# Optimization experiments

Hardware: AMD Instinct MI355X
Metric: run time of the kernel (lower is better)

## Reference

```python
import jax, jax.numpy as jnp
import numpy as np

E = 1024   # embedding_dim
H = 16     # heads
W = 1024   # lag / seq length
B = 4      # batch
D = E // H # head dim


def setup_inputs() -> dict:
    key = jax.random.key(0)
    ks = jax.random.split(key, 5)
    scale = E ** -0.5
    return {
        "x":   jax.random.normal(ks[0], (3, B, E, W), dtype=jnp.float32),
        "L_Q": jax.random.normal(ks[1], (E, E), dtype=jnp.float32) * scale,
        "L_K": jax.random.normal(ks[2], (E, E), dtype=jnp.float32) * scale,
        "L_V": jax.random.normal(ks[3], (E, E), dtype=jnp.float32) * scale,
        "M":   jax.random.normal(ks[4], (E, E), dtype=jnp.float32) * (1.0 / (2 * E)) ** 0.5,
        "b":   jnp.zeros((E, 1), dtype=jnp.float32),
    }


def reference(x, L_Q, L_K, L_V, M, b):
    # x: [3, B, E, W] channels-first; x[0]=K input, x[1]=Q input, x[2]=V input
    K = jnp.einsum('ef,bfw->bew', L_K, x[0])
    Q = jnp.einsum('ef,bfw->bew', L_Q, x[1])
    V = jnp.einsum('ef,bfw->bew', L_V, x[2])
    # reshape to [B, H, D, W]
    Kv = K.reshape(B, H, D, W)
    Qv = Q.reshape(B, H, D, W)
    Vv = V.reshape(B, H, D, W)
    # scores[b,h,q,k] = Q_v^T @ K_v
    scores = jnp.einsum('bhdq,bhdk->bhqk', Qv, Kv)
    # causal mask: -inf for q > k (strictly lower triangle), added BEFORE softmax
    q_idx = jnp.arange(W)[:, None]
    k_idx = jnp.arange(W)[None, :]
    mask = jnp.where(q_idx > k_idx, -jnp.inf, 0.0).astype(scores.dtype)
    scores = scores + mask
    # NON-STANDARD: softmax over the QUERY axis (dim=-2), then scale
    attn = jax.nn.softmax(scores, axis=-2) / (E ** 0.5)
    # V_v @ scores: [B,H,D,W] @ [B,H,W,W] -> [B,H,D,W]
    out = jnp.einsum('bhdq,bhqk->bhdk', Vv, attn).reshape(B, E, W)
    # dense: M @ out + b (dropout identity at inference)
    return jnp.einsum('oe,bew->bow', M, out) + b
```

## Files before the change

### kernel.cpp

```cpp
#include <hip/hip_runtime.h>
#include <stdint.h>
#include <math.h>

#define E_DIM 1024
#define W_DIM 1024
#define EW 1048576L

typedef _Float16 h16;
typedef __attribute__((ext_vector_type(8))) _Float16 h8;
typedef __attribute__((ext_vector_type(4))) float f4;

__device__ __forceinline__ void async_copy16(h16* lds, const h16* g) {
    __builtin_amdgcn_global_load_lds(
        (const __attribute__((address_space(1))) void*)g,
        (__attribute__((address_space(3))) void*)lds, 16, 0, 0);
}

__global__ __launch_bounds__(256) void prep(
    const float* __restrict__ x, const float* __restrict__ LK,
    const float* __restrict__ LQ, const float* __restrict__ LV,
    const float* __restrict__ Mw, h16* __restrict__ xt, h16* __restrict__ wh)
{
    __shared__ float Ts[64][65];
    const int z = blockIdx.z;
    const int t = threadIdx.x;
    if (z < 12) {
        const float* src = x + (long)z * EW;
        h16* dst = xt + (long)z * EW;
        const int e0 = blockIdx.y * 64, w0 = blockIdx.x * 64;
        const int r = t >> 4, c4 = (t & 15) * 4;
        #pragma unroll
        for (int p = 0; p < 4; ++p) {
            float4 v = *reinterpret_cast<const float4*>(src + (long)(e0 + r + p * 16) * W_DIM + w0 + c4);
            Ts[c4 + 0][r + p * 16] = v.x;
            Ts[c4 + 1][r + p * 16] = v.y;
            Ts[c4 + 2][r + p * 16] = v.z;
            Ts[c4 + 3][r + p * 16] = v.w;
        }
        __syncthreads();
        const int r2 = t >> 3, c8 = (t & 7) * 8;
        #pragma unroll
        for (int p = 0; p < 2; ++p) {
            int wr = r2 + p * 32;
            union { h16 h[8]; uint4 u; } o;
            #pragma unroll
            for (int k = 0; k < 8; ++k) o.h[k] = (h16)Ts[wr][c8 + k];
            *reinterpret_cast<uint4*>(dst + (long)(w0 + wr) * E_DIM + e0 + c8) = o.u;
        }
    } else {
        const float* srcs[4] = {LK, LQ, LV, Mw};
        const float* s = srcs[z - 12];
        h16* o = wh + (long)(z - 12) * EW;
        long base = ((long)(blockIdx.y * 16 + blockIdx.x)) * 1024 + t;
        #pragma unroll
        for (int k = 0; k < 4; ++k) {
            long i = base + k * 256;
            float4 v = reinterpret_cast<const float4*>(s)[i];
            union { h16 h[4]; uint2 u; } u;
            u.h[0] = (h16)v.x; u.h[1] = (h16)v.y; u.h[2] = (h16)v.z; u.h[3] = (h16)v.w;
            reinterpret_cast<uint2*>(o)[i] = u.u;
        }
    }
}

__global__ __launch_bounds__(512) void gemm_proj3(
    const h16* __restrict__ xh, const h16* __restrict__ Wts,
    h16* __restrict__ KQV)
{
    __shared__ h16 As[4][256 * 32];
    __shared__ h16 Bs[4][256 * 32];

    const int t = threadIdx.x;
    const int wave = t >> 6, lane = t & 63;
    const int quad = lane >> 4, l16 = lane & 15;
    const int mi = wave >> 2, ni = wave & 3;
    const int wm = mi * 128, wn = ni * 64;

    const int lin = (int)blockIdx.x + ((int)blockIdx.y << 2) + ((int)blockIdx.z << 4);
    const int swz = (lin & 7) * 24 + (lin >> 3);
    const int bx = swz & 3, by = (swz >> 2) & 3, zz = swz >> 4;

    const int m0 = by * 256, n0 = bx * 256;

    const int proj = zz >> 2, bz = zz & 3;
    const h16 *A, *Bt; h16* C;
    if (proj == 0)      { A = xh + bz * EW;       Bt = Wts;          C = KQV + bz * EW; }
    else if (proj == 1) { A = xh + (4 + bz) * EW; Bt = Wts + EW;     C = KQV + (4 + bz) * EW; }
    else                { A = Wts + 2 * EW;       Bt = xh + (8 + bz) * EW; C = KQV + (8 + bz) * EW; }

    f4 acc[8][4] = {};

    auto stageA = [&](int buf, int k0) {
        #pragma unroll
        for (int j = 0; j < 2; ++j) {
            int g = j * 512 + t, row = g >> 2, cg = (g & 3) ^ ((row >> 1) & 3);
            async_copy16(&As[buf][g * 8], A + (long)(m0 + row) * E_DIM + k0 + cg * 8);
        }
    };
    auto stageB = [&](int buf, int k0) {
        #pragma unroll
        for (int j = 0; j < 2; ++j) {
            int g = j * 512 + t, row = g >> 2, cg = (g & 3) ^ ((row >> 1) & 3);
            async_copy16(&Bs[buf][g * 8], Bt + (long)(n0 + row) * E_DIM + k0 + cg * 8);
        }
    };

    stageA(0, 0);  stageB(0, 0);
    stageA(1, 32); stageB(1, 32);
    stageA(2, 64); stageB(2, 64);
    asm volatile("s_waitcnt vmcnt(8)" ::: "memory");
    __builtin_amdgcn_s_barrier();

    for (int H = 0; H < 32; ++H) {
        const h16* as = As[H & 3];
        const h16* bs = Bs[H & 3];
        const int kn = (H + 3) * 32;
        const bool st = (H + 3) < 32;

        h8 bv[4], av[4];
        #pragma unroll
        for (int j = 0; j < 4; ++j) {
            int rb = wn + j * 16 + l16;
            bv[j] = *reinterpret_cast<const h8*>(&bs[(rb * 4 + (quad ^ ((rb >> 1) & 3))) * 8]);
        }
        #pragma unroll
        for (int i = 0; i < 4; ++i) {
            int ra = wm + i * 16 + l16;
            av[i] = *reinterpret_cast<const h8*>(&as[(ra * 4 + (quad ^ ((ra >> 1) & 3))) * 8]);
        }
        if (st) stageA((H + 3) & 3, kn);
        __builtin_amdgcn_s_barrier();
        __builtin_amdgcn_s_setprio(1);
        #pragma unroll
        for (int i = 0; i < 4; ++i)
            #pragma unroll
            for (int j = 0; j < 4; ++j)
                acc[i][j] = __builtin_amdgcn_mfma_f32_16x16x32_f16(av[i], bv[j], acc[i][j], 0, 0, 0);
        __builtin_amdgcn_s_setprio(0);
        __builtin_amdgcn_s_barrier();

        #pragma unroll
        for (int i = 0; i < 4; ++i) {
            int ra = wm + 64 + i * 16 + l16;
            av[i] = *reinterpret_cast<const h8*>(&as[(ra * 4 + (quad ^ ((ra >> 1) & 3))) * 8]);
        }
        if (st) stageB((H + 3) & 3, kn);
        if (H < 29)       asm volatile("s_waitcnt vmcnt(8)" ::: "memory");
        else if (H == 29) asm volatile("s_waitcnt vmcnt(4)" ::: "memory");
        else if (H == 30) asm volatile("s_waitcnt vmcnt(0)" ::: "memory");
        __builtin_amdgcn_s_barrier();
        __builtin_amdgcn_s_setprio(1);
        #pragma unroll
        for (int i = 0; i < 4; ++i)
            #pragma unroll
            for (int j = 0; j < 4; ++j)
                acc[4 + i][j] = __builtin_amdgcn_mfma_f32_16x16x32_f16(av[i], bv[j], acc[4 + i][j], 0, 0, 0);
        __builtin_amdgcn_s_setprio(0);
        __builtin_amdgcn_s_barrier();
    }

    #pragma unroll
    for (int mt = 0; mt < 8; ++mt)
        #pragma unroll
        for (int i = 0; i < 4; ++i) {
            int m = m0 + wm + mt * 16 + quad * 4 + i;
            #pragma unroll
            for (int nt = 0; nt < 4; ++nt)
                C[(long)m * W_DIM + n0 + wn + nt * 16 + l16] = (h16)acc[mt][nt][i];
        }
}

__global__ __launch_bounds__(256) void gemm_out(
    const h16* __restrict__ A, const h16* __restrict__ Bt,
    float* __restrict__ C, const float* __restrict__ bias)
{
    __shared__ h16 As[64 * 64];
    __shared__ h16 Bs[128 * 64];

    const int t = threadIdx.x;
    const int wave = t >> 6, lane = t & 63;
    const int quad = lane >> 4, l16 = lane & 15;
    const int m0 = blockIdx.y * 64, n0 = blockIdx.x * 128;
    const int wm = (wave >> 1) * 32, wn = (wave & 1) * 64;

    f4 acc[2][4] = {};

    for (int k0 = 0; k0 < 1024; k0 += 64) {
        __syncthreads();
        #pragma unroll
        for (int j = 0; j < 2; ++j) {
            int g = j * 256 + t, row = g >> 3, cg = (g & 7) ^ (row & 7);
            async_copy16(&As[g * 8], A + (long)(m0 + row) * E_DIM + k0 + cg * 8);
        }
        #pragma unroll
        for (int j = 0; j < 4; ++j) {
            int g = j * 256 + t, row = g >> 3, cg = (g & 7) ^ (row & 7);
            async_copy16(&Bs[g * 8], Bt + (long)(n0 + row) * E_DIM + k0 + cg * 8);
        }
        __syncthreads();

        h8 av[2][2], bv[4][2];
        #pragma unroll
        for (int c = 0; c < 2; ++c) {
            #pragma unroll
            for (int mt = 0; mt < 2; ++mt) {
                int r = wm + mt * 16 + l16;
                av[mt][c] = *reinterpret_cast<const h8*>(&As[(r * 8 + ((c * 4 + quad) ^ (l16 & 7))) * 8]);
            }
            #pragma unroll
            for (int nt = 0; nt < 4; ++nt) {
                int r = wn + nt * 16 + l16;
                bv[nt][c] = *reinterpret_cast<const h8*>(&Bs[(r * 8 + ((c * 4 + quad) ^ (l16 & 7))) * 8]);
            }
        }
        #pragma unroll
        for (int c = 0; c < 2; ++c)
            #pragma unroll
            for (int mt = 0; mt < 2; ++mt)
                #pragma unroll
                for (int nt = 0; nt < 4; ++nt)
                    acc[mt][nt] = __builtin_amdgcn_mfma_f32_16x16x32_f16(av[mt][c], bv[nt][c], acc[mt][nt], 0, 0, 0);
    }

    #pragma unroll
    for (int mt = 0; mt < 2; ++mt)
        #pragma unroll
        for (int i = 0; i < 4; ++i) {
            int m = m0 + wm + mt * 16 + quad * 4 + i;
            float bv_ = bias ? bias[m] : 0.f;
            #pragma unroll
            for (int nt = 0; nt < 4; ++nt) {
                int n = n0 + wn + nt * 16 + l16;
                C[(long)(n >> 10) * EW + (long)m * W_DIM + (n & 1023)] = acc[mt][nt][i] + bv_;
            }
        }
}

__global__ __launch_bounds__(512) void attn_mfma(
    const h16* __restrict__ Kt, const h16* __restrict__ Qt,
    const h16* __restrict__ V, h16* __restrict__ AoT)
{
    __shared__ h16 Qs[2][2][64 * 64];
    __shared__ h16 Vs[2][2][64 * 64];
    __shared__ h16 Ps[8][16 * 64];

    const int t = threadIdx.x, wave = t >> 6, lane = t & 63;
    const int quad = lane >> 4, l16 = lane & 15;
    const int y = blockIdx.y;
    const int b = y >> 4, h = y & 15;
    const int cxor = (y & 7) ^ (((y >> 5) & 1) ? 7 : 0);
    const int ktb = (int)blockIdx.x ^ cxor;
    const int nit = ktb + 1;
    const int kwave = ktb * 128 + wave * 16;
    const int kc = kwave + l16;

    const h16* Ktb_ = Kt + (long)b * EW + h * 64;
    const h16* Qtb  = Qt + (long)b * EW + h * 64;
    const h16* Vb   = V  + (long)b * EW + (long)(h * 64) * W_DIM;
    h16* Pw = &Ps[wave][0];

    h8 kb0 = *reinterpret_cast<const h8*>(Ktb_ + (long)kc * E_DIM + quad * 8);
    h8 kb1 = *reinterpret_cast<const h8*>(Ktb_ + (long)kc * E_DIM + 32 + quad * 8);

    const int srow = t >> 3, scg = (t & 7) ^ (srow & 7);
    #pragma unroll
    for (int hs = 0; hs < 2; ++hs) {
        async_copy16(&Qs[0][hs][t * 8], Qtb + (long)(hs * 64 + srow) * E_DIM + scg * 8);
        async_copy16(&Vs[0][hs][t * 8], Vb + (long)srow * W_DIM + hs * 64 + scg * 8);
    }

    const float L2E = 1.442695041f;
    float mr = -1e30f, ls = 0.f;
    f4 O[4] = {};

    for (int it = 0; it < nit; ++it) {
        const int q0 = it * 128;
        __syncthreads();
        if (it + 1 < nit) {
            const int nb = (it + 1) & 1, q1 = q0 + 128;
            #pragma unroll
            for (int hs = 0; hs < 2; ++hs) {
                async_copy16(&Qs[nb][hs][t * 8], Qtb + (long)(q1 + hs * 64 + srow) * E_DIM + scg * 8);
                async_copy16(&Vs[nb][hs][t * 8], Vb + (long)srow * W_DIM + q1 + hs * 64 + scg * 8);
            }
        }

        for (int sub = 0; sub < 2; ++sub) {
            const int q0s = q0 + sub * 64;
            if (q0s > kwave + 15) continue;

            const h16* qs = &Qs[it & 1][sub][0];
            const h16* vs = &Vs[it & 1][sub][0];

            f4 S[4];
            __builtin_amdgcn_s_setprio(1);
            #pragma unroll
            for (int nt = 0; nt < 4; ++nt) {
                int row = nt * 16 + l16;
                h8 a0 = *reinterpret_cast<const h8*>(&qs[(row * 8 + (quad ^ (l16 & 7))) * 8]);
                h8 a1 = *reinterpret_cast<const h8*>(&qs[(row * 8 + ((4 + quad) ^ (l16 & 7))) * 8]);
                f4 s = {};
                s = __builtin_amdgcn_mfma_f32_16x16x32_f16(a0, kb0, s, 0, 0, 0);
                s = __builtin_amdgcn_mfma_f32_16x16x32_f16(a1, kb1, s, 0, 0, 0);
                S[nt] = s;
            }
            __builtin_amdgcn_s_setprio(0);

            if (2 * it + sub >= 2 * ktb) {
                #pragma unroll
                for (int nt = 0; nt < 4; ++nt)
                    #pragma unroll
                    for (int i = 0; i < 4; ++i)
                        if (q0s + nt * 16 + quad * 4 + i > kc) S[nt][i] = -1e30f;
            }

            float mx = -1e30f;
            #pragma unroll
            for (int nt = 0; nt < 4; ++nt) {
                float t0 = fmaxf(fmaxf(S[nt][0], S[nt][1]), fmaxf(S[nt][2], S[nt][3]));
                mx = fmaxf(mx, t0);
            }
            mx = fmaxf(mx, __shfl_xor(mx, 16));
            mx = fmaxf(mx, __shfl_xor(mx, 32));

            if (__any(mx - mr > 8.f)) {
                float nm = fmaxf(mr, mx);
                float al = exp2f((mr - nm) * L2E);
                mr = nm;
                ls *= al;
                #pragma unroll
                for (int dt = 0; dt < 4; ++dt)
                    #pragma unroll
                    for (int i = 0; i < 4; ++i) O[dt][i] *= al;
            }

            const float mc = mr * L2E;
            float tsa = 0.f, tsb = 0.f;
            #pragma unroll
            for (int nt = 0; nt < 4; ++nt)
                #pragma unroll
                for (int i = 0; i < 4; ++i) {
                    float p = exp2f(fmaf(S[nt][i], L2E, -mc));
                    S[nt][i] = p;
                    if (i & 1) tsb += p; else tsa += p;
                }
            float ts = tsa + tsb;
            ts += __shfl_xor(ts, 16);
            ts += __shfl_xor(ts, 32);
            ls += ts;

            #pragma unroll
            for (int nt = 0; nt < 4; ++nt) {
                int sg = ((nt * 2 + (quad >> 1)) ^ (l16 & 7)) * 8 + (quad & 1) * 4;
                union { h16 hh[4]; uint2 u2; } u0;
                #pragma unroll
                for (int i = 0; i < 4; ++i) u0.hh[i] = (h16)S[nt][i];
                *reinterpret_cast<uint2*>(Pw + l16 * 64 + sg) = u0.u2;
            }
            asm volatile("" ::: "memory");

            __builtin_amdgcn_s_setprio(1);
            #pragma unroll
            for (int c = 0; c < 2; ++c) {
                int sg = ((c * 4 + quad) ^ (l16 & 7)) * 8;
                h8 pb = *reinterpret_cast<const h8*>(Pw + l16 * 64 + sg);
                #pragma unroll
                for (int dt = 0; dt < 4; ++dt) {
                    int r = dt * 16 + l16;
                    h8 va = *reinterpret_cast<const h8*>(&vs[(r * 8 + ((c * 4 + quad) ^ (l16 & 7))) * 8]);
                    O[dt] = __builtin_amdgcn_mfma_f32_16x16x32_f16(va, pb, O[dt], 0, 0, 0);
                }
            }
            __builtin_amdgcn_s_setprio(0);
            asm volatile("" ::: "memory");
        }
    }

    const float inv = 0.03125f / ls;
    #pragma unroll
    for (int dt = 0; dt < 4; ++dt) {
        int sg = ((dt * 2 + (quad >> 1)) ^ (l16 & 7)) * 8 + (quad & 1) * 4;
        union { h16 hh[4]; uint2 u2; } u0;
        #pragma unroll
        for (int i = 0; i < 4; ++i) u0.hh[i] = (h16)(O[dt][i] * inv);
        *reinterpret_cast<uint2*>(Pw + l16 * 64 + sg) = u0.u2;
    }
    asm volatile("" ::: "memory");
    #pragma unroll
    for (int j = 0; j < 2; ++j) {
        int sg = ((quad * 2 + j) ^ (l16 & 7)) * 8;
        uint4 vv = *reinterpret_cast<const uint4*>(Pw + l16 * 64 + sg);
        *reinterpret_cast<uint4*>(AoT + (long)b * EW + (long)(kwave + l16) * E_DIM
                                  + h * 64 + quad * 16 + j * 8) = vv;
    }
}

extern "C" void kernel_launch(void* const* d_in, const int* in_sizes, int n_in,
                              void* d_out, int out_size, void* d_ws, size_t ws_size,
                              hipStream_t stream)
{
    const float* x  = (const float*)d_in[0];
    const float* LQ = (const float*)d_in[1];
    const float* LK = (const float*)d_in[2];
    const float* LV = (const float*)d_in[3];
    const float* Mw = (const float*)d_in[4];
    const float* bb = (const float*)d_in[5];
    float* out = (float*)d_out;
    h16* ws = (h16*)d_ws;

    h16* xh  = ws;
    h16* LKh = ws + 12 * EW;
    h16* Mh  = ws + 15 * EW;
    h16* Kp  = ws + 16 * EW;
    h16* Qp  = ws + 20 * EW;
    h16* Vp  = ws + 24 * EW;
    h16* Ao  = ws + 28 * EW;

    dim3 blk(256);
    prep<<<dim3(16, 16, 16), blk, 0, stream>>>(x, LK, LQ, LV, Mw, xh, LKh);
    gemm_proj3<<<dim3(4, 4, 12), dim3(512), 0, stream>>>(xh, LKh, Kp);
    attn_mfma<<<dim3(8, 64), dim3(512), 0, stream>>>(Kp, Qp, Vp, Ao);
    gemm_out<<<dim3(32, 16), blk, 0, stream>>>(Mh, Ao, out, bb);
}
```

Measured before the change: 186.4 us.

## Load B operand and V tiles directly from global into registers, bypassing LDS

New measurement: 251.6 us. 35.0% more time.

```diff
diff --git a/kernel.cpp b/kernel.cpp
--- a/kernel.cpp
+++ b/kernel.cpp
@@ -68,7 +68,6 @@
     h16* __restrict__ KQV)
 {
     __shared__ h16 As[4][256 * 32];
-    __shared__ h16 Bs[4][256 * 32];
 
     const int t = threadIdx.x;
     const int wave = t >> 6, lane = t & 63;
@@ -97,65 +96,49 @@
             async_copy16(&As[buf][g * 8], A + (long)(m0 + row) * E_DIM + k0 + cg * 8);
         }
     };
-    auto stageB = [&](int buf, int k0) {
-        #pragma unroll
-        for (int j = 0; j < 2; ++j) {
-            int g = j * 512 + t, row = g >> 2, cg = (g & 3) ^ ((row >> 1) & 3);
-            async_copy16(&Bs[buf][g * 8], Bt + (long)(n0 + row) * E_DIM + k0 + cg * 8);
-        }
+    auto loadB = [&](h8* dst, int k0) {
+        #pragma unroll
+        for (int j = 0; j < 4; ++j)
+            dst[j] = *reinterpret_cast<const h8*>(
+                Bt + (long)(n0 + wn + j * 16 + l16) * E_DIM + k0 + quad * 8);
     };
 
-    stageA(0, 0);  stageB(0, 0);
-    stageA(1, 32); stageB(1, 32);
-    stageA(2, 64); stageB(2, 64);
-    asm volatile("s_waitcnt vmcnt(8)" ::: "memory");
+    h8 bvc[4], bvn[4];
+    loadB(bvc, 0);
+    __builtin_amdgcn_sched_barrier(0);
+    stageA(0, 0);
+    stageA(1, 32);
+    stageA(2, 64);
+    asm volatile("s_waitcnt vmcnt(4)" ::: "memory");
     __builtin_amdgcn_s_barrier();
 
     for (int H = 0; H < 32; ++H) {
         const h16* as = As[H & 3];
-        const h16* bs = Bs[H & 3];
-        const int kn = (H + 3) * 32;
-        const bool st = (H + 3) < 32;
-
-        h8 bv[4], av[4];
-        #pragma unroll
-        for (int j = 0; j < 4; ++j) {
-            int rb = wn + j * 16 + l16;
-            bv[j] = *reinterpret_cast<const h8*>(&bs[(rb * 4 + (quad ^ ((rb >> 1) & 3))) * 8]);
-        }
-        #pragma unroll
-        for (int i = 0; i < 4; ++i) {
+
+        if (H + 1 < 32) loadB(bvn, (H + 1) * 32);
+        __builtin_amdgcn_sched_barrier(0);
+        if (H + 3 < 32) stageA((H + 3) & 3, (H + 3) * 32);
+        __builtin_amdgcn_sched_barrier(0);
+        if (H <= 28)      asm volatile("s_waitcnt vmcnt(8)" ::: "memory");
+        else if (H == 29) asm volatile("s_waitcnt vmcnt(6)" ::: "memory");
+        else if (H == 30) asm volatile("s_waitcnt vmcnt(4)" ::: "memory");
+        else              asm volatile("s_waitcnt vmcnt(0)" ::: "memory");
+
+        h8 av[8];
+        #pragma unroll
+        for (int i = 0; i < 8; ++i) {
             int ra = wm + i * 16 + l16;
             av[i] = *reinterpret_cast<const h8*>(&as[(ra * 4 + (quad ^ ((ra >> 1) & 3))) * 8]);
         }
-        if (st) stageA((H + 3) & 3, kn);
-        __builtin_amdgcn_s_barrier();
         __builtin_amdgcn_s_setprio(1);
         #pragma unroll
-        for (int i = 0; i < 4; ++i)
+        for (int i = 0; i < 8; ++i)
             #pragma unroll
             for (int j = 0; j < 4; ++j)
-                acc[i][j] = __builtin_amdgcn_mfma_f32_16x16x32_f16(av[i], bv[j], acc[i][j], 0, 0, 0);
+                acc[i][j] = __builtin_amdgcn_mfma_f32_16x16x32_f16(av[i], bvc[j], acc[i][j], 0, 0, 0);
         __builtin_amdgcn_s_setprio(0);
-        __builtin_amdgcn_s_barrier();
-
-        #pragma unroll
-        for (int i = 0; i < 4; ++i) {
-            int ra = wm + 64 + i * 16 + l16;
-            av[i] = *reinterpret_cast<const h8*>(&as[(ra * 4 + (quad ^ ((ra >> 1) & 3))) * 8]);
-        }
-        if (st) stageB((H + 3) & 3, kn);
-        if (H < 29)       asm volatile("s_waitcnt vmcnt(8)" ::: "memory");
-        else if (H == 29) asm volatile("s_waitcnt vmcnt(4)" ::: "memory");
-        else if (H == 30) asm volatile("s_waitcnt vmcnt(0)" ::: "memory");
-        __builtin_amdgcn_s_barrier();
-        __builtin_amdgcn_s_setprio(1);
-        #pragma unroll
-        for (int i = 0; i < 4; ++i)
-            #pragma unroll
-            for (int j = 0; j < 4; ++j)
-                acc[4 + i][j] = __builtin_amdgcn_mfma_f32_16x16x32_f16(av[i], bv[j], acc[4 + i][j], 0, 0, 0);
-        __builtin_amdgcn_s_setprio(0);
+        #pragma unroll
+        for (int j = 0; j < 4; ++j) bvc[j] = bvn[j];
         __builtin_amdgcn_s_barrier();
     }
 
@@ -241,7 +224,6 @@
     const h16* __restrict__ V, h16* __restrict__ AoT)
 {
     __shared__ h16 Qs[2][2][64 * 64];
-    __shared__ h16 Vs[2][2][64 * 64];
     __shared__ h16 Ps[8][16 * 64];
 
     const int t = threadIdx.x, wave = t >> 6, lane = t & 63;
@@ -264,10 +246,8 @@
 
     const int srow = t >> 3, scg = (t & 7) ^ (srow & 7);
     #pragma unroll
-    for (int hs = 0; hs < 2; ++hs) {
+    for (int hs = 0; hs < 2; ++hs)
         async_copy16(&Qs[0][hs][t * 8], Qtb + (long)(hs * 64 + srow) * E_DIM + scg * 8);
-        async_copy16(&Vs[0][hs][t * 8], Vb + (long)srow * W_DIM + hs * 64 + scg * 8);
-    }
 
     const float L2E = 1.442695041f;
     float mr = -1e30f, ls = 0.f;
@@ -279,10 +259,8 @@
         if (it + 1 < nit) {
             const int nb = (it + 1) & 1, q1 = q0 + 128;
             #pragma unroll
-            for (int hs = 0; hs < 2; ++hs) {
+            for (int hs = 0; hs < 2; ++hs)
                 async_copy16(&Qs[nb][hs][t * 8], Qtb + (long)(q1 + hs * 64 + srow) * E_DIM + scg * 8);
-                async_copy16(&Vs[nb][hs][t * 8], Vb + (long)srow * W_DIM + q1 + hs * 64 + scg * 8);
-            }
         }
 
         for (int sub = 0; sub < 2; ++sub) {
@@ -290,7 +268,14 @@
             if (q0s > kwave + 15) continue;
 
             const h16* qs = &Qs[it & 1][sub][0];
-            const h16* vs = &Vs[it & 1][sub][0];
+
+            h8 va[4][2];
+            #pragma unroll
+            for (int dt = 0; dt < 4; ++dt)
+                #pragma unroll
+                for (int c = 0; c < 2; ++c)
+                    va[dt][c] = *reinterpret_cast<const h8*>(
+                        Vb + (long)(dt * 16 + l16) * W_DIM + q0s + c * 32 + quad * 8);
 
             f4 S[4];
             __builtin_amdgcn_s_setprio(1);
@@ -365,11 +350,8 @@
                 int sg = ((c * 4 + quad) ^ (l16 & 7)) * 8;
                 h8 pb = *reinterpret_cast<const h8*>(Pw + l16 * 64 + sg);
                 #pragma unroll
-                for (int dt = 0; dt < 4; ++dt) {
-                    int r = dt * 16 + l16;
-                    h8 va = *reinterpret_cast<const h8*>(&vs[(r * 8 + ((c * 4 + quad) ^ (l16 & 7))) * 8]);
-                    O[dt] = __builtin_amdgcn_mfma_f32_16x16x32_f16(va, pb, O[dt], 0, 0, 0);
-                }
+                for (int dt = 0; dt < 4; ++dt)
+                    O[dt] = __builtin_amdgcn_mfma_f32_16x16x32_f16(va[dt][c], pb, O[dt], 0, 0, 0);
             }
             __builtin_amdgcn_s_setprio(0);
             asm volatile("" ::: "memory");
```
